# Kernel tuning notes

Hardware: AMD Instinct MI355X
Metric: run time of the kernel (lower is better)

The kernel has to match this reference:

```python
import jax, jax.numpy as jnp
import numpy as np

NUM_PERIODS = 24


def setup_inputs() -> dict:
    key = jax.random.key(0)
    ks = jax.random.split(key, 12)
    B, N, D_IN, D_OUT, H, E = 32, 2000, 32, 32, 64, 16
    # static adjacency mask: sparse-ish nonneg weights (the torch module stores ADJ_MX sparse,
    # densifies it, and multiplies elementwise)
    adj = jax.random.uniform(ks[0], (N, N), dtype=jnp.float32)
    adj = jnp.where(adj > 0.95, adj, 0.0)
    scale = lambda d: 1.0 / np.sqrt(d)
    return {
        "input_features": jax.random.normal(ks[1], (B, N, D_IN), dtype=jnp.float32),
        "cycle_indices": jax.random.randint(ks[2], (B,), 0, 168),
        "adj_static": adj,
        "env_features": jax.random.normal(ks[3], (N, E), dtype=jnp.float32),
        "W_env": jax.random.normal(ks[4], (E, H), dtype=jnp.float32) * scale(E),
        "b_env": jnp.zeros((H,), dtype=jnp.float32),
        "src_emb": jax.random.normal(ks[5], (NUM_PERIODS, N, H), dtype=jnp.float32) * scale(H),
        "tgt_emb": jax.random.normal(ks[6], (NUM_PERIODS, N, H), dtype=jnp.float32) * scale(H),
        "weight": jax.random.normal(ks[7], (D_IN, D_OUT), dtype=jnp.float32) * scale(D_IN),
        "bias": jnp.zeros((D_OUT,), dtype=jnp.float32),
        "W_res": jax.random.normal(ks[8], (D_IN, D_OUT), dtype=jnp.float32) * scale(D_IN),
        "b_res": jnp.zeros((D_OUT,), dtype=jnp.float32),
    }


def reference(input_features, cycle_indices, adj_static, env_features, W_env, b_env,
              src_emb, tgt_emb, weight, bias, W_res, b_res):
    # eval mode: all dropouts are identity
    # environmental encoder: Linear + ReLU  -> [N, H]
    env = jax.nn.relu(env_features @ W_env + b_env)
    # adaptive adjacency for every period: relu((S+E)(T+E)^T) * static_mask  -> [P, N, N]
    S = src_emb + env[None]
    T = tgt_emb + env[None]
    A = jax.nn.relu(jnp.einsum('pnh,pmh->pnm', S, T)) * adj_static[None]
    # map each batch sample to its period's adjacency (replaces the torch per-period loop)
    periods = cycle_indices % NUM_PERIODS          # [B]
    support = jnp.einsum('bnd,dm->bnm', input_features, weight)  # [B, N, M]
    conv = jnp.einsum('bnk,bkm->bnm', A[periods], support) + bias
    residual = jax.nn.relu(input_features @ W_res + b_res)
    return jax.nn.relu(conv + residual)
```

## Files before the change

### kernel.cpp

```cpp
#include <hip/hip_runtime.h>
#include <hip/hip_bf16.h>
#include <cstdint>

#define NN 2000
#define NNP 2048
#define NB 32
#define DD 32
#define HH 64
#define EE 16
#define NP 24
#define NT 32
#define KSPLIT 2
#define KITERS (NNP / 64 / KSPLIT)
#define LSTR 68

typedef _Float16 f16;
typedef _Float16 half8 __attribute__((ext_vector_type(8)));
typedef _Float16 half4v __attribute__((ext_vector_type(4)));
typedef float f32x4 __attribute__((ext_vector_type(4)));

__global__ __launch_bounds__(64) void k_prep(const float* __restrict__ envf,
                                             const float* __restrict__ Wenv,
                                             const float* __restrict__ benv,
                                             const float* __restrict__ src,
                                             const float* __restrict__ tgt,
                                             f16* __restrict__ Sb,
                                             f16* __restrict__ Tb) {
    int n = blockIdx.x, h = threadIdx.x;
    if (n >= NN) {
        for (int p = 0; p < NP; ++p) {
            size_t o = ((size_t)n * NP + p) * HH + h;
            Sb[o] = (f16)0.f; Tb[o] = (f16)0.f;
        }
        return;
    }
    float acc = benv[h];
#pragma unroll
    for (int e = 0; e < EE; ++e) acc = fmaf(envf[n * EE + e], Wenv[e * HH + h], acc);
    acc = fmaxf(acc, 0.f);
    for (int p = 0; p < NP; ++p) {
        size_t i = ((size_t)p * NN + n) * HH + h;
        size_t o = ((size_t)n * NP + p) * HH + h;
        Sb[o] = (f16)(src[i] + acc);
        Tb[o] = (f16)(tgt[i] + acc);
    }
}

__global__ __launch_bounds__(256) void k_suppT(const float* __restrict__ x,
                                               const float* __restrict__ W,
                                               const float* __restrict__ Wres,
                                               const float* __restrict__ bres,
                                               f16* __restrict__ suppT,
                                               float* __restrict__ resd) {
    __shared__ float w[DD * DD], wr[DD * DD];
    for (int i = threadIdx.x; i < DD * DD; i += 256) { w[i] = W[i]; wr[i] = Wres[i]; }
    __syncthreads();
    int idx = blockIdx.x * 256 + threadIdx.x;
    int b = idx >> 11, node = idx & (NNP - 1);
    if (node >= NN) {
#pragma unroll
        for (int m = 0; m < DD; ++m) suppT[((size_t)b * DD + m) * NNP + node] = (f16)0.f;
        return;
    }
    float xv[DD];
    const float4* xr = (const float4*)(x + ((size_t)b * NN + node) * DD);
#pragma unroll
    for (int q = 0; q < DD / 4; ++q) {
        float4 v = xr[q];
        xv[4 * q] = v.x; xv[4 * q + 1] = v.y; xv[4 * q + 2] = v.z; xv[4 * q + 3] = v.w;
    }
    float sa[DD], ra[DD];
#pragma unroll
    for (int m = 0; m < DD; ++m) { sa[m] = 0.f; ra[m] = bres[m]; }
#pragma unroll
    for (int d = 0; d < DD; ++d) {
        float xd = xv[d];
#pragma unroll
        for (int m = 0; m < DD; ++m) {
            sa[m] = fmaf(xd, w[d * DD + m], sa[m]);
            ra[m] = fmaf(xd, wr[d * DD + m], ra[m]);
        }
    }
#pragma unroll
    for (int m = 0; m < DD; ++m)
        suppT[((size_t)b * DD + m) * NNP + node] = (f16)sa[m];
    float4* ro = (float4*)(resd + ((size_t)b * NN + node) * DD);
#pragma unroll
    for (int q = 0; q < DD / 4; ++q)
        ro[q] = make_float4(fmaxf(ra[4 * q], 0.f), fmaxf(ra[4 * q + 1], 0.f),
                            fmaxf(ra[4 * q + 2], 0.f), fmaxf(ra[4 * q + 3], 0.f));
}

__global__ __launch_bounds__(256) void k_conv2(const f16* __restrict__ Sb,
                                               const f16* __restrict__ Tb,
                                               const f16* __restrict__ suppT,
                                               const float* __restrict__ adj,
                                               const int* __restrict__ cyc,
                                               float* __restrict__ accbuf) {
    int bi = blockIdx.x;
    int b = bi & 31;
    int ks = (bi >> 5) & (KSPLIT - 1);
    int nt = bi >> 6;
    int p = cyc[b] % NP; if (p < 0) p += NP;

    __shared__ f16 Tt[64][LSTR];
    __shared__ f16 Pt[64][LSTR];
    __shared__ f16 Sup[DD][LSTR];

    int t = threadIdx.x;
    int w = t >> 6, l = t & 63;
    int u = l & 15, g = l >> 4;
    int wm = w * 16;
    int n0 = nt * 64;

    const f16* sbase = Sb + ((size_t)(n0 + wm + u) * NP + p) * HH + 8 * g;
    half8 af0 = *(const half8*)(sbase);
    half8 af1 = *(const half8*)(sbase + 32);

    f32x4 acc0 = (f32x4){0.f, 0.f, 0.f, 0.f};
    f32x4 acc1 = (f32x4){0.f, 0.f, 0.f, 0.f};

    for (int kl = 0; kl < KITERS; ++kl) {
        int k0 = (ks * KITERS + kl) * 64;
        float av[4][4];
#pragma unroll
        for (int cc = 0; cc < 4; ++cc) {
            int kcol = k0 + 16 * cc + u;
#pragma unroll
            for (int r = 0; r < 4; ++r) {
                int nrow = n0 + wm + 4 * g + r;
                av[cc][r] = (nrow < NN && kcol < NN) ? adj[(size_t)nrow * NN + kcol] : 0.f;
            }
        }
        __syncthreads();
        {
            int row = t >> 2, ch = t & 3;
            const half4v* gp = (const half4v*)(Tb + ((size_t)(k0 + row) * NP + p) * HH + ch * 16);
            half4v v0 = gp[0], v1 = gp[1], v2 = gp[2], v3 = gp[3];
            *(half4v*)&Tt[row][ch * 16]      = v0;
            *(half4v*)&Tt[row][ch * 16 + 4]  = v1;
            *(half4v*)&Tt[row][ch * 16 + 8]  = v2;
            *(half4v*)&Tt[row][ch * 16 + 12] = v3;
        }
        {
            int m = t >> 3, ch = t & 7;
            const half4v* gp = (const half4v*)(suppT + ((size_t)b * DD + m) * NNP + k0 + ch * 8);
            half4v v0 = gp[0], v1 = gp[1];
            *(half4v*)&Sup[m][ch * 8] = v0;
            *(half4v*)&Sup[m][ch * 8 + 4] = v1;
        }
        __syncthreads();
#pragma unroll
        for (int cc = 0; cc < 4; ++cc) {
            half4v b0lo = *(const half4v*)&Tt[16 * cc + u][8 * g];
            half4v b0hi = *(const half4v*)&Tt[16 * cc + u][8 * g + 4];
            half4v b1lo = *(const half4v*)&Tt[16 * cc + u][32 + 8 * g];
            half4v b1hi = *(const half4v*)&Tt[16 * cc + u][32 + 8 * g + 4];
            half8 bf0 = {b0lo[0], b0lo[1], b0lo[2], b0lo[3], b0hi[0], b0hi[1], b0hi[2], b0hi[3]};
            half8 bf1 = {b1lo[0], b1lo[1], b1lo[2], b1lo[3], b1hi[0], b1hi[1], b1hi[2], b1hi[3]};
            f32x4 pacc = (f32x4){0.f, 0.f, 0.f, 0.f};
            pacc = __builtin_amdgcn_mfma_f32_16x16x32_f16(af0, bf0, pacc, 0, 0, 0);
            pacc = __builtin_amdgcn_mfma_f32_16x16x32_f16(af1, bf1, pacc, 0, 0, 0);
#pragma unroll
            for (int r = 0; r < 4; ++r)
                Pt[wm + 4 * g + r][16 * cc + u] = (f16)(fmaxf(pacc[r], 0.f) * av[cc][r]);
        }
        __syncthreads();
#pragma unroll
        for (int s = 0; s < 2; ++s) {
            half4v plo = *(const half4v*)&Pt[wm + u][32 * s + 8 * g];
            half4v phi = *(const half4v*)&Pt[wm + u][32 * s + 8 * g + 4];
            half8 paf = {plo[0], plo[1], plo[2], plo[3], phi[0], phi[1], phi[2], phi[3]};
            {
                half4v slo = *(const half4v*)&Sup[u][32 * s + 8 * g];
                half4v shi = *(const half4v*)&Sup[u][32 * s + 8 * g + 4];
                half8 sbf = {slo[0], slo[1], slo[2], slo[3], shi[0], shi[1], shi[2], shi[3]};
                acc0 = __builtin_amdgcn_mfma_f32_16x16x32_f16(paf, sbf, acc0, 0, 0, 0);
            }
            {
                half4v slo = *(const half4v*)&Sup[16 + u][32 * s + 8 * g];
                half4v shi = *(const half4v*)&Sup[16 + u][32 * s + 8 * g + 4];
                half8 sbf = {slo[0], slo[1], slo[2], slo[3], shi[0], shi[1], shi[2], shi[3]};
                acc1 = __builtin_amdgcn_mfma_f32_16x16x32_f16(paf, sbf, acc1, 0, 0, 0);
            }
        }
    }
#pragma unroll
    for (int r = 0; r < 4; ++r) {
        int nrow = n0 + wm + 4 * g + r;
        size_t o = ((size_t)b * NNP + nrow) * DD + u;
        atomicAdd(&accbuf[o], acc0[r]);
        atomicAdd(&accbuf[o + 16], acc1[r]);
    }
}

__global__ __launch_bounds__(256) void k_fin(const float* __restrict__ accbuf,
                                             const float* __restrict__ resd,
                                             const float* __restrict__ bias,
                                             float* __restrict__ out) {
    int idx = blockIdx.x * 256 + threadIdx.x;
    if (idx >= NB * NN * (DD / 4)) return;
    int m4 = idx & 7;
    int n = (idx >> 3) % NN;
    int b = idx / (NN * 8);
    float4 a = ((const float4*)accbuf)[((size_t)b * NNP + n) * 8 + m4];
    float4 rs = ((const float4*)resd)[(size_t)idx];
    float4 bv = ((const float4*)bias)[m4];
    float4 o = make_float4(fmaxf(a.x + bv.x + rs.x, 0.f), fmaxf(a.y + bv.y + rs.y, 0.f),
                           fmaxf(a.z + bv.z + rs.z, 0.f), fmaxf(a.w + bv.w + rs.w, 0.f));
    ((float4*)out)[(size_t)idx] = o;
}

extern "C" void kernel_launch(void* const* d_in, const int* in_sizes, int n_in,
                              void* d_out, int out_size, void* d_ws, size_t ws_size,
                              hipStream_t stream) {
    const float* x    = (const float*)d_in[0];
    const int*   cyc  = (const int*)d_in[1];
    const float* adj  = (const float*)d_in[2];
    const float* envf = (const float*)d_in[3];
    const float* Wenv = (const float*)d_in[4];
    const float* benv = (const float*)d_in[5];
    const float* src  = (const float*)d_in[6];
    const float* tgt  = (const float*)d_in[7];
    const float* W    = (const float*)d_in[8];
    const float* bias = (const float*)d_in[9];
    const float* Wres = (const float*)d_in[10];
    const float* bres = (const float*)d_in[11];
    float* out = (float*)d_out;
    char* ws = (char*)d_ws;

    f16*   Sb     = (f16*)(ws + 0);
    f16*   Tb     = (f16*)(ws + 6291456);
    f16*   suppT  = (f16*)(ws + 12582912);
    float* resd   = (float*)(ws + 16777216);
    float* accbuf = (float*)(ws + 24969216);

    hipMemsetAsync(accbuf, 0, (size_t)NB * NNP * DD * 4, stream);
    hipLaunchKernelGGL(k_prep, dim3(NNP), dim3(HH), 0, stream,
                       envf, Wenv, benv, src, tgt, Sb, Tb);
    hipLaunchKernelGGL(k_suppT, dim3(NB * NNP / 256), dim3(256), 0, stream,
                       x, W, Wres, bres, suppT, resd);
    hipLaunchKernelGGL(k_conv2, dim3(NT * KSPLIT * NB), dim3(256), 0, stream,
                       Sb, Tb, suppT, adj, cyc, accbuf);
    hipLaunchKernelGGL(k_fin, dim3((NB * NN * (DD / 4) + 255) / 256), dim3(256), 0, stream,
                       accbuf, resd, bias, out);
}
```

Measured before the change: 200.8 us.

## Merge prep kernels with memset, raise K-split, prefetch conv tiles into registers

Result: slower. 205.1 us (+2.1%).

```diff
diff --git a/kernel.cpp b/kernel.cpp
--- a/kernel.cpp
+++ b/kernel.cpp
@@ -10,85 +10,90 @@
 #define EE 16
 #define NP 24
 #define NT 32
-#define KSPLIT 2
+#define KSPLIT 4
 #define KITERS (NNP / 64 / KSPLIT)
-#define LSTR 68
+#define LSTR 72
 
 typedef _Float16 f16;
 typedef _Float16 half8 __attribute__((ext_vector_type(8)));
-typedef _Float16 half4v __attribute__((ext_vector_type(4)));
 typedef float f32x4 __attribute__((ext_vector_type(4)));
 
-__global__ __launch_bounds__(64) void k_prep(const float* __restrict__ envf,
+__global__ __launch_bounds__(256) void k_pre(const float* __restrict__ envf,
                                              const float* __restrict__ Wenv,
                                              const float* __restrict__ benv,
                                              const float* __restrict__ src,
                                              const float* __restrict__ tgt,
+                                             const float* __restrict__ x,
+                                             const float* __restrict__ W,
+                                             const float* __restrict__ Wres,
+                                             const float* __restrict__ bres,
                                              f16* __restrict__ Sb,
-                                             f16* __restrict__ Tb) {
-    int n = blockIdx.x, h = threadIdx.x;
-    if (n >= NN) {
+                                             f16* __restrict__ Tb,
+                                             f16* __restrict__ suppT,
+                                             float* __restrict__ resd,
+                                             float* __restrict__ accbuf) {
+    int blk = blockIdx.x, t = threadIdx.x;
+    if (blk < 512) {
+        int n = blk * 4 + (t >> 6), h = t & 63;
+        if (n >= NN) {
+            for (int p = 0; p < NP; ++p) {
+                size_t o = ((size_t)n * NP + p) * HH + h;
+                Sb[o] = (f16)0.f; Tb[o] = (f16)0.f;
+            }
+            return;
+        }
+        float acc = benv[h];
+#pragma unroll
+        for (int e = 0; e < EE; ++e) acc = fmaf(envf[n * EE + e], Wenv[e * HH + h], acc);
+        acc = fmaxf(acc, 0.f);
         for (int p = 0; p < NP; ++p) {
+            size_t i = ((size_t)p * NN + n) * HH + h;
             size_t o = ((size_t)n * NP + p) * HH + h;
-            Sb[o] = (f16)0.f; Tb[o] = (f16)0.f;
-        }
-        return;
-    }
-    float acc = benv[h];
-#pragma unroll
-    for (int e = 0; e < EE; ++e) acc = fmaf(envf[n * EE + e], Wenv[e * HH + h], acc);
-    acc = fmaxf(acc, 0.f);
-    for (int p = 0; p < NP; ++p) {
-        size_t i = ((size_t)p * NN + n) * HH + h;
-        size_t o = ((size_t)n * NP + p) * HH + h;
-        Sb[o] = (f16)(src[i] + acc);
-        Tb[o] = (f16)(tgt[i] + acc);
-    }
-}
-
-__global__ __launch_bounds__(256) void k_suppT(const float* __restrict__ x,
-                                               const float* __restrict__ W,
-                                               const float* __restrict__ Wres,
-                                               const float* __restrict__ bres,
-                                               f16* __restrict__ suppT,
-                                               float* __restrict__ resd) {
-    __shared__ float w[DD * DD], wr[DD * DD];
-    for (int i = threadIdx.x; i < DD * DD; i += 256) { w[i] = W[i]; wr[i] = Wres[i]; }
-    __syncthreads();
-    int idx = blockIdx.x * 256 + threadIdx.x;
-    int b = idx >> 11, node = idx & (NNP - 1);
-    if (node >= NN) {
-#pragma unroll
-        for (int m = 0; m < DD; ++m) suppT[((size_t)b * DD + m) * NNP + node] = (f16)0.f;
-        return;
-    }
-    float xv[DD];
-    const float4* xr = (const float4*)(x + ((size_t)b * NN + node) * DD);
-#pragma unroll
-    for (int q = 0; q < DD / 4; ++q) {
-        float4 v = xr[q];
-        xv[4 * q] = v.x; xv[4 * q + 1] = v.y; xv[4 * q + 2] = v.z; xv[4 * q + 3] = v.w;
-    }
-    float sa[DD], ra[DD];
-#pragma unroll
-    for (int m = 0; m < DD; ++m) { sa[m] = 0.f; ra[m] = bres[m]; }
-#pragma unroll
-    for (int d = 0; d < DD; ++d) {
-        float xd = xv[d];
-#pragma unroll
-        for (int m = 0; m < DD; ++m) {
-            sa[m] = fmaf(xd, w[d * DD + m], sa[m]);
-            ra[m] = fmaf(xd, wr[d * DD + m], ra[m]);
-        }
-    }
-#pragma unroll
-    for (int m = 0; m < DD; ++m)
-        suppT[((size_t)b * DD + m) * NNP + node] = (f16)sa[m];
-    float4* ro = (float4*)(resd + ((size_t)b * NN + node) * DD);
-#pragma unroll
-    for (int q = 0; q < DD / 4; ++q)
-        ro[q] = make_float4(fmaxf(ra[4 * q], 0.f), fmaxf(ra[4 * q + 1], 0.f),
-                            fmaxf(ra[4 * q + 2], 0.f), fmaxf(ra[4 * q + 3], 0.f));
+            Sb[o] = (f16)(src[i] + acc);
+            Tb[o] = (f16)(tgt[i] + acc);
+        }
+    } else if (blk < 768) {
+        __shared__ float w[DD * DD], wr[DD * DD];
+        for (int i = t; i < DD * DD; i += 256) { w[i] = W[i]; wr[i] = Wres[i]; }
+        __syncthreads();
+        int idx = (blk - 512) * 256 + t;
+        int b = idx >> 11, node = idx & (NNP - 1);
+        if (node >= NN) {
+#pragma unroll
+            for (int m = 0; m < DD; ++m) suppT[((size_t)b * DD + m) * NNP + node] = (f16)0.f;
+            return;
+        }
+        float xv[DD];
+        const float4* xr = (const float4*)(x + ((size_t)b * NN + node) * DD);
+#pragma unroll
+        for (int q = 0; q < DD / 4; ++q) {
+            float4 v = xr[q];
+            xv[4 * q] = v.x; xv[4 * q + 1] = v.y; xv[4 * q + 2] = v.z; xv[4 * q + 3] = v.w;
+        }
+        float sa[DD], ra[DD];
+#pragma unroll
+        for (int m = 0; m < DD; ++m) { sa[m] = 0.f; ra[m] = bres[m]; }
+#pragma unroll
+        for (int d = 0; d < DD; ++d) {
+            float xd = xv[d];
+#pragma unroll
+            for (int m = 0; m < DD; ++m) {
+                sa[m] = fmaf(xd, w[d * DD + m], sa[m]);
+                ra[m] = fmaf(xd, wr[d * DD + m], ra[m]);
+            }
+        }
+#pragma unroll
+        for (int m = 0; m < DD; ++m)
+            suppT[((size_t)b * DD + m) * NNP + node] = (f16)sa[m];
+        float4* ro = (float4*)(resd + ((size_t)b * NN + node) * DD);
+#pragma unroll
+        for (int q = 0; q < DD / 4; ++q)
+            ro[q] = make_float4(fmaxf(ra[4 * q], 0.f), fmaxf(ra[4 * q + 1], 0.f),
+                                fmaxf(ra[4 * q + 2], 0.f), fmaxf(ra[4 * q + 3], 0.f));
+    } else {
+        int i = (blk - 768) * 256 + t;
+        ((float4*)accbuf)[i] = make_float4(0.f, 0.f, 0.f, 0.f);
+    }
 }
 
 __global__ __launch_bounds__(256) void k_conv2(const f16* __restrict__ Sb,
@@ -100,7 +105,7 @@
     int bi = blockIdx.x;
     int b = bi & 31;
     int ks = (bi >> 5) & (KSPLIT - 1);
-    int nt = bi >> 6;
+    int nt = bi >> 7;
     int p = cyc[b] % NP; if (p < 0) p += NP;
 
     __shared__ f16 Tt[64][LSTR];
@@ -117,47 +122,62 @@
     half8 af0 = *(const half8*)(sbase);
     half8 af1 = *(const half8*)(sbase + 32);
 
+    const float* arow[4];
+    float rowm[4];
+#pragma unroll
+    for (int r = 0; r < 4; ++r) {
+        int nrow = n0 + wm + 4 * g + r;
+        rowm[r] = (nrow < NN) ? 1.f : 0.f;
+        arow[r] = adj + (size_t)(nrow < NN ? nrow : 0) * NN;
+    }
+
+    int srow = t >> 2, sch = t & 3;
+    int sm = t >> 3, sch2 = t & 7;
+    const f16* tb_ptr  = Tb + ((size_t)(ks * KITERS * 64 + srow) * NP + p) * HH + sch * 16;
+    const f16* sup_ptr = suppT + ((size_t)b * DD + sm) * NNP + ks * KITERS * 64 + sch2 * 8;
+
     f32x4 acc0 = (f32x4){0.f, 0.f, 0.f, 0.f};
     f32x4 acc1 = (f32x4){0.f, 0.f, 0.f, 0.f};
+
+    half8 rt0 = *(const half8*)(tb_ptr);
+    half8 rt1 = *(const half8*)(tb_ptr + 8);
+    half8 rs0 = *(const half8*)(sup_ptr);
 
     for (int kl = 0; kl < KITERS; ++kl) {
         int k0 = (ks * KITERS + kl) * 64;
         float av[4][4];
+        if (k0 + 64 <= NN) {
+#pragma unroll
+            for (int cc = 0; cc < 4; ++cc) {
+                int kcol = k0 + 16 * cc + u;
+#pragma unroll
+                for (int r = 0; r < 4; ++r) av[cc][r] = rowm[r] * arow[r][kcol];
+            }
+        } else {
+#pragma unroll
+            for (int cc = 0; cc < 4; ++cc) {
+                int kcol = k0 + 16 * cc + u;
+#pragma unroll
+                for (int r = 0; r < 4; ++r)
+                    av[cc][r] = (kcol < NN) ? rowm[r] * arow[r][kcol] : 0.f;
+            }
+        }
+        __syncthreads();
+        *(half8*)&Tt[srow][sch * 16]     = rt0;
+        *(half8*)&Tt[srow][sch * 16 + 8] = rt1;
+        *(half8*)&Sup[sm][sch2 * 8]      = rs0;
+        __syncthreads();
+        if (kl + 1 < KITERS) {
+            tb_ptr  += (size_t)64 * NP * HH;
+            sup_ptr += 64;
+            rt0 = *(const half8*)(tb_ptr);
+            rt1 = *(const half8*)(tb_ptr + 8);
+            rs0 = *(const half8*)(sup_ptr);
+        }
 #pragma unroll
         for (int cc = 0; cc < 4; ++cc) {
-            int kcol = k0 + 16 * cc + u;
-#pragma unroll
-            for (int r = 0; r < 4; ++r) {
-                int nrow = n0 + wm + 4 * g + r;
-                av[cc][r] = (nrow < NN && kcol < NN) ? adj[(size_t)nrow * NN + kcol] : 0.f;
-            }
-        }
-        __syncthreads();
-        {
-            int row = t >> 2, ch = t & 3;
-            const half4v* gp = (const half4v*)(Tb + ((size_t)(k0 + row) * NP + p) * HH + ch * 16);
-            half4v v0 = gp[0], v1 = gp[1], v2 = gp[2], v3 = gp[3];
-            *(half4v*)&Tt[row][ch * 16]      = v0;
-            *(half4v*)&Tt[row][ch * 16 + 4]  = v1;
-            *(half4v*)&Tt[row][ch * 16 + 8]  = v2;
-            *(half4v*)&Tt[row][ch * 16 + 12] = v3;
-        }
-        {
-            int m = t >> 3, ch = t & 7;
-            const half4v* gp = (const half4v*)(suppT + ((size_t)b * DD + m) * NNP + k0 + ch * 8);
-            half4v v0 = gp[0], v1 = gp[1];
-            *(half4v*)&Sup[m][ch * 8] = v0;
-            *(half4v*)&Sup[m][ch * 8 + 4] = v1;
-        }
-        __syncthreads();
-#pragma unroll
-        for (int cc = 0; cc < 4; ++cc) {
-            half4v b0lo = *(const half4v*)&Tt[16 * cc + u][8 * g];
-            half4v b0hi = *(const half4v*)&Tt[16 * cc + u][8 * g + 4];
-            half4v b1lo = *(const half4v*)&Tt[16 * cc + u][32 + 8 * g];
-            half4v b1hi = *(const half4v*)&Tt[16 * cc + u][32 + 8 * g + 4];
-            half8 bf0 = {b0lo[0], b0lo[1], b0lo[2], b0lo[3], b0hi[0], b0hi[1], b0hi[2], b0hi[3]};
-            half8 bf1 = {b1lo[0], b1lo[1], b1lo[2], b1lo[3], b1hi[0], b1hi[1], b1hi[2], b1hi[3]};
+            half8 bf0 = *(const half8*)&Tt[16 * cc + u][8 * g];
+            half8 bf1 = *(const half8*)&Tt[16 * cc + u][32 + 8 * g];
             f32x4 pacc = (f32x4){0.f, 0.f, 0.f, 0.f};
             pacc = __builtin_amdgcn_mfma_f32_16x16x32_f16(af0, bf0, pacc, 0, 0, 0);
             pacc = __builtin_amdgcn_mfma_f32_16x16x32_f16(af1, bf1, pacc, 0, 0, 0);
@@ -168,21 +188,11 @@
         __syncthreads();
 #pragma unroll
         for (int s = 0; s < 2; ++s) {
-            half4v plo = *(const half4v*)&Pt[wm + u][32 * s + 8 * g];
-            half4v phi = *(const half4v*)&Pt[wm + u][32 * s + 8 * g + 4];
-            half8 paf = {plo[0], plo[1], plo[2], plo[3], phi[0], phi[1], phi[2], phi[3]};
-            {
-                half4v slo = *(const half4v*)&Sup[u][32 * s + 8 * g];
-                half4v shi = *(const half4v*)&Sup[u][32 * s + 8 * g + 4];
-                half8 sbf = {slo[0], slo[1], slo[2], slo[3], shi[0], shi[1], shi[2], shi[3]};
-                acc0 = __builtin_amdgcn_mfma_f32_16x16x32_f16(paf, sbf, acc0, 0, 0, 0);
-            }
-            {
-                half4v slo = *(const half4v*)&Sup[16 + u][32 * s + 8 * g];
-                half4v shi = *(const half4v*)&Sup[16 + u][32 * s + 8 * g + 4];
-                half8 sbf = {slo[0], slo[1], slo[2], slo[3], shi[0], shi[1], shi[2], shi[3]};
-                acc1 = __builtin_amdgcn_mfma_f32_16x16x32_f16(paf, sbf, acc1, 0, 0, 0);
-            }
+            half8 paf  = *(const half8*)&Pt[wm + u][32 * s + 8 * g];
+            half8 sbf0 = *(const half8*)&Sup[u][32 * s + 8 * g];
+            half8 sbf1 = *(const half8*)&Sup[16 + u][32 * s + 8 * g];
+            acc0 = __builtin_amdgcn_mfma_f32_16x16x32_f16(paf, sbf0, acc0, 0, 0, 0);
+            acc1 = __builtin_amdgcn_mfma_f32_16x16x32_f16(paf, sbf1, acc1, 0, 0, 0);
         }
     }
 #pragma unroll
@@ -235,11 +245,9 @@
     float* resd   = (float*)(ws + 16777216);
     float* accbuf = (float*)(ws + 24969216);
 
-    hipMemsetAsync(accbuf, 0, (size_t)NB * NNP * DD * 4, stream);
-    hipLaunchKernelGGL(k_prep, dim3(NNP), dim3(HH), 0, stream,
-                       envf, Wenv, benv, src, tgt, Sb, Tb);
-    hipLaunchKernelGGL(k_suppT, dim3(NB * NNP / 256), dim3(256), 0, stream,
-                       x, W, Wres, bres, suppT, resd);
+    hipLaunchKernelGGL(k_pre, dim3(2816), dim3(256), 0, stream,
+                       envf, Wenv, benv, src, tgt, x, W, Wres, bres,
+                       Sb, Tb, suppT, resd, accbuf);
     hipLaunchKernelGGL(k_conv2, dim3(NT * KSPLIT * NB), dim3(256), 0, stream,
                        Sb, Tb, suppT, adj, cyc, accbuf);
     hipLaunchKernelGGL(k_fin, dim3((NB * NN * (DD / 4) + 255) / 256), dim3(256), 0, stream,
```
